# Optimization experiments

Measured on AMD Instinct MI355X. Metric: run time of the kernel, lower is better.

The kernel has to match this reference:

```python
import jax, jax.numpy as jnp
import numpy as np

H = 512
L = 4
A = 16
EPS = 1e-5


def setup_inputs() -> dict:
    key = jax.random.key(0)
    ks = jax.random.split(key, 16)
    B, S = 64, 256
    scale = 0.02
    inp = {
        "hidden": jnp.zeros((B, H), jnp.float32),
        "x": jax.random.normal(ks[0], (B, S, H), jnp.float32),
        "dones": jax.random.randint(ks[1], (B, S), 0, 2).astype(bool),
        "avail_actions": jax.random.randint(ks[2], (B, S, A), 0, 2).astype(bool),
        # MLP stack: L layers of Linear(H,H) + LayerNorm
        "Wl": jax.random.normal(ks[3], (L, H, H), jnp.float32) * scale,
        "bl": jnp.zeros((L, H), jnp.float32),
        "ln_g": jnp.ones((L, H), jnp.float32),
        "ln_b": jnp.zeros((L, H), jnp.float32),
        # GRUCell(H, H): torch layout weight_ih [3H, H] (r, z, n order)
        "W_ih": jax.random.normal(ks[4], (3 * H, H), jnp.float32) * scale,
        "W_hh": jax.random.normal(ks[5], (3 * H, H), jnp.float32) * scale,
        "b_ih": jnp.zeros((3 * H,), jnp.float32),
        "b_hh": jnp.zeros((3 * H,), jnp.float32),
        # output head
        "Wq": jax.random.normal(ks[6], (A, H), jnp.float32) * scale,
        "bq": jnp.zeros((A,), jnp.float32),
    }
    return inp


def _layer_norm(x, g, b):
    mu = jnp.mean(x, axis=-1, keepdims=True)
    var = jnp.mean(jnp.square(x - mu), axis=-1, keepdims=True)
    return (x - mu) * jax.lax.rsqrt(var + EPS) * g + b


def _gru_scan(h0, x, dones, W_ih, W_hh, b_ih, b_hh):
    # Precompute input projections for all timesteps: [B, S, 3H]
    gi = jnp.einsum("bsh,gh->bsg", x, W_ih) + b_ih
    gi_t = jnp.swapaxes(gi, 0, 1)          # [S, B, 3H]
    dones_t = jnp.swapaxes(dones, 0, 1)    # [S, B]

    def step(h, inputs):
        gi_s, done_s = inputs
        h = jnp.where(done_s[:, None], 0.0, h)  # reset carry where done
        gh = h @ W_hh.T + b_hh
        i_r, i_z, i_n = jnp.split(gi_s, 3, axis=-1)
        h_r, h_z, h_n = jnp.split(gh, 3, axis=-1)
        r = jax.nn.sigmoid(i_r + h_r)
        z = jax.nn.sigmoid(i_z + h_z)
        n = jnp.tanh(i_n + r * h_n)
        h_new = (1.0 - z) * n + z * h
        return h_new, h_new

    h_final, outs = jax.lax.scan(step, h0, (gi_t, dones_t))
    return h_final, jnp.swapaxes(outs, 0, 1)  # [B, S, H]


def reference(hidden, x, dones, avail_actions, Wl, bl, ln_g, ln_b,
              W_ih, W_hh, b_ih, b_hh, Wq, bq):
    h = x
    for l in range(L):
        h = jnp.einsum("bsh,oh->bso", h, Wl[l]) + bl[l]
        h = jax.nn.relu(_layer_norm(h, ln_g[l], ln_b[l]))
    hidden_out, rnn_out = _gru_scan(hidden, h, dones, W_ih, W_hh, b_ih, b_hh)
    q = jnp.einsum("bsh,ah->bsa", rnn_out, Wq) + bq
    unavail = 1.0 - avail_actions.astype(q.dtype)
    q = q - unavail * 1e10
    return hidden_out, q
```

## Files before the change

### kernel.cpp

```cpp
#include <hip/hip_runtime.h>
#include <hip/hip_bf16.h>

typedef short short8 __attribute__((ext_vector_type(8)));
typedef float f32x4 __attribute__((ext_vector_type(4)));

#define H 512
#define BATCH 64
#define SEQ 256
#define NROWS 16384
#define NDOM 16
#define HSTCAP 12288

__device__ __forceinline__ float bf2f(unsigned short u) {
    union { unsigned int i; float f; } v;
    v.i = ((unsigned int)u) << 16;
    return v.f;
}
__device__ __forceinline__ unsigned short f2bf(float f) {
    union { float f; unsigned int i; } v;
    v.f = f;
    unsigned int lsb = (v.i >> 16) & 1u;
    v.i += 0x7fffu + lsb;
    return (unsigned short)(v.i >> 16);
}
__device__ __forceinline__ float sigm(float x) { return 1.f / (1.f + __expf(-x)); }
__device__ __forceinline__ float tanh_fast(float x) { return 2.f / (1.f + __expf(-2.f * x)) - 1.f; }

__global__ __launch_bounds__(256) void cvt_init(
    const float* __restrict__ Wl, const float* __restrict__ Wih,
    unsigned short* __restrict__ wlb, unsigned short* __restrict__ wihb,
    unsigned int* __restrict__ meta)
{
    long idx4 = (long)blockIdx.x * 256 + threadIdx.x;
    if (idx4 < 20480) meta[idx4] = 0u;
    long i = idx4 * 4;
    const long N1 = 1048576;
    const long N2 = N1 + 786432;
    const float* src; unsigned short* dst; long off;
    if (i < N1)      { src = Wl;  dst = wlb;  off = i; }
    else if (i < N2) { src = Wih; dst = wihb; off = i - N1; }
    else return;
    float4 v = *(const float4*)(src + off);
    ushort4 o;
    o.x = f2bf(v.x); o.y = f2bf(v.y); o.z = f2bf(v.z); o.w = f2bf(v.w);
    *(ushort4*)(dst + off) = o;
}

__global__ __launch_bounds__(256) void seg_build(
    const int* __restrict__ dones, int* __restrict__ lenArr,
    unsigned int* __restrict__ hist)
{
    __shared__ int d[256];
    const int b = blockIdx.x, s = threadIdx.x;
    d[s] = dones[b * 256 + s];
    __syncthreads();
    int len = 0;
    bool start = (s == 0) || (d[s] != 0);
    if (start) {
        len = 1;
        while (s + len < 256 && d[s + len] == 0) len++;
        atomicAdd(&hist[len], 1u);
    }
    lenArr[b * 256 + s] = len;
}

__global__ __launch_bounds__(256) void seg_offsets(
    const unsigned int* __restrict__ hist, int* __restrict__ Marr,
    unsigned int* __restrict__ offs, unsigned int* __restrict__ ssum)
{
    __shared__ unsigned int h[257];
    __shared__ int Msh[257];
    const int t = threadIdx.x;
    h[t] = hist[t];
    if (t == 0) h[256] = hist[256];
    __syncthreads();
    for (int tt = t; tt <= 256; tt += 256) {
        unsigned int m = 0;
        for (int L = tt + 1; L <= 256; ++L) m += h[L];
        Marr[tt] = (int)m;
        offs[tt] = m;
        Msh[tt] = (int)m;
    }
    __syncthreads();
    if (t == 0) {
        unsigned int acc = 0;
        for (int k = 0; k <= 256; ++k) { ssum[k] = acc; acc += (unsigned int)Msh[k]; }
    }
}

__global__ __launch_bounds__(256) void seg_scatter(
    const int* __restrict__ lenArr, unsigned int* __restrict__ offs,
    int* __restrict__ recs)
{
    const int b = blockIdx.x, s = threadIdx.x;
    int len = lenArr[b * 256 + s];
    if (len > 0) {
        unsigned int pos = atomicAdd(&offs[len], 1u);
        recs[pos] = (b << 16) | s;
    }
}

__global__ __launch_bounds__(256) void pmap_build(
    const int* __restrict__ recs, const int* __restrict__ Marr,
    const unsigned int* __restrict__ ssum, const int* __restrict__ lenArr,
    int* __restrict__ pmap)
{
    const int i = blockIdx.x * 256 + threadIdx.x;
    if (i >= Marr[0]) return;
    int rec = recs[i];
    int b = rec >> 16, st = rec & 0xffff;
    int len = lenArr[b * 256 + st];
    for (int t = 0; t < len; ++t) pmap[b * 256 + st + t] = (int)ssum[t] + i;
}

__global__ __launch_bounds__(256) void h_init(
    const int* __restrict__ recs, const int* __restrict__ Marr,
    const int* __restrict__ dones, const float* __restrict__ hidden,
    unsigned short* __restrict__ hst)
{
    const int w = threadIdx.x >> 6, lane = threadIdx.x & 63;
    const int i = blockIdx.x * 4 + w;
    const int nseg = Marr[0];
    const int c0 = lane * 8;
    unsigned short* dst = hst + (long)i * 512 + c0;
    if (i < nseg) {
        int rec = recs[i];
        int b = rec >> 16, st = rec & 0xffff;
        if (st == 0 && dones[b * 256] == 0) {
            float4 va = *(const float4*)(hidden + b * 512 + c0);
            float4 vb = *(const float4*)(hidden + b * 512 + c0 + 4);
            ushort4 o0 = {f2bf(va.x), f2bf(va.y), f2bf(va.z), f2bf(va.w)};
            ushort4 o1 = {f2bf(vb.x), f2bf(vb.y), f2bf(vb.z), f2bf(vb.w)};
            *(ushort4*)dst = o0; *(ushort4*)(dst + 4) = o1;
            return;
        }
    }
    ushort4 z4 = {0, 0, 0, 0};
    *(ushort4*)dst = z4; *(ushort4*)(dst + 4) = z4;
}

__global__ __launch_bounds__(256, 2) void mlp_gi(
    const float* __restrict__ x,
    const unsigned short* __restrict__ wlb,
    const unsigned short* __restrict__ wihb,
    const float* __restrict__ bl,
    const float* __restrict__ lng,
    const float* __restrict__ lnb,
    const float* __restrict__ bih,
    const int* __restrict__ pmap,
    unsigned short* __restrict__ gi)
{
    __shared__ unsigned short ldsAct[32 * 512];
    __shared__ unsigned short ldsW[512 * 32];
    __shared__ float red[32 * 8];
    const int tid = threadIdx.x;
    const int lane = tid & 63;
    const int w = tid >> 6;
    const long m0 = (long)blockIdx.x * 32;
    const int l15 = lane & 15;
    const int l4 = lane >> 4;

    int stSrc[8];
    unsigned int* stDst[8];
#pragma unroll
    for (int i = 0; i < 8; ++i) {
        int o = (i * 256 + tid) * 16;
        int row = o >> 6;
        int ch = (o & 63) >> 4;
        int sw = (row & 3) ^ ((row >> 2) & 3);
        stSrc[i] = row * 1024 + ((ch ^ sw) << 4);
        stDst[i] = (unsigned int*)(ldsW + (i * 256 + w * 64) * 8);
    }
    int afBase[2], afSw[2];
#pragma unroll
    for (int i = 0; i < 2; ++i) {
        int arow = i * 16 + l15;
        afBase[i] = arow * 1024 + l4 * 16;
        afSw[i] = (arow & 7) << 4;
    }
    int bfOff[8];
#pragma unroll
    for (int jn = 0; jn < 8; ++jn) {
        int wrow = w * 128 + jn * 16 + l15;
        int sw = (wrow & 3) ^ ((wrow >> 2) & 3);
        bfOff[jn] = wrow * 64 + ((l4 ^ sw) << 4);
    }

#pragma unroll
    for (int it = 0; it < 8; ++it) {
        int ch = it * 256 + tid;
        int row = ch >> 6;
        int c = ch & 63;
        const float* xp = x + (m0 + row) * 512 + c * 8;
        float4 a = *(const float4*)xp;
        float4 b4 = *(const float4*)(xp + 4);
        short8 v;
        v[0] = (short)f2bf(a.x);  v[1] = (short)f2bf(a.y);
        v[2] = (short)f2bf(a.z);  v[3] = (short)f2bf(a.w);
        v[4] = (short)f2bf(b4.x); v[5] = (short)f2bf(b4.y);
        v[6] = (short)f2bf(b4.z); v[7] = (short)f2bf(b4.w);
        int byteo = (row * 1024 + c * 16) ^ ((row & 7) << 4);
        *(short8*)((char*)ldsAct + byteo) = v;
    }
    __syncthreads();

    for (int u = 0; u < 7; ++u) {
        const char* Wb = (u < 4) ? (const char*)(wlb + (long)u * 262144)
                                 : (const char*)(wihb + (long)(u - 4) * 262144);
        f32x4 acc[2][8];
#pragma unroll
        for (int i = 0; i < 2; ++i)
#pragma unroll
            for (int jn = 0; jn < 8; ++jn) acc[i][jn] = (f32x4){0.f, 0.f, 0.f, 0.f};

        for (int kt = 0; kt < 16; ++kt) {
            const int ktb = kt * 64;
            __syncthreads();
#pragma unroll
            for (int i = 0; i < 8; ++i)
                __builtin_amdgcn_global_load_lds(
                    (const unsigned int*)(Wb + stSrc[i] + ktb), stDst[i], 16, 0, 0);
            __syncthreads();

            short8 af[2], bfr[8];
#pragma unroll
            for (int i = 0; i < 2; ++i)
                af[i] = *(const short8*)((const char*)ldsAct + ((afBase[i] + ktb) ^ afSw[i]));
#pragma unroll
            for (int jn = 0; jn < 8; ++jn)
                bfr[jn] = *(const short8*)((const char*)ldsW + bfOff[jn]);
            __builtin_amdgcn_s_setprio(1);
#pragma unroll
            for (int i = 0; i < 2; ++i)
#pragma unroll
                for (int jn = 0; jn < 8; ++jn)
                    acc[i][jn] = __builtin_amdgcn_mfma_f32_16x16x32_bf16(af[i], bfr[jn], acc[i][jn], 0, 0, 0);
            __builtin_amdgcn_s_setprio(0);
        }

        if (u < 4) {
            float bz[8], gl[8], bb[8];
#pragma unroll
            for (int jn = 0; jn < 8; ++jn) {
                int n = w * 128 + jn * 16 + l15;
                bz[jn] = bl[u * 512 + n]; gl[jn] = lng[u * 512 + n]; bb[jn] = lnb[u * 512 + n];
            }
#pragma unroll
            for (int i = 0; i < 2; ++i)
#pragma unroll
                for (int jn = 0; jn < 8; ++jn)
#pragma unroll
                    for (int r = 0; r < 4; ++r) acc[i][jn][r] += bz[jn];

#pragma unroll
            for (int i = 0; i < 2; ++i) {
#pragma unroll
                for (int r = 0; r < 4; ++r) {
                    float sv = 0.f, qv = 0.f;
#pragma unroll
                    for (int jn = 0; jn < 8; ++jn) {
                        float v = acc[i][jn][r];
                        sv += v; qv += v * v;
                    }
                    sv += __shfl_xor(sv, 1); qv += __shfl_xor(qv, 1);
                    sv += __shfl_xor(sv, 2); qv += __shfl_xor(qv, 2);
                    sv += __shfl_xor(sv, 4); qv += __shfl_xor(qv, 4);
                    sv += __shfl_xor(sv, 8); qv += __shfl_xor(qv, 8);
                    if (l15 == 0) {
                        int row = i * 16 + l4 * 4 + r;
                        red[row * 8 + w * 2] = sv;
                        red[row * 8 + w * 2 + 1] = qv;
                    }
                }
            }
            __syncthreads();

#pragma unroll
            for (int i = 0; i < 2; ++i) {
#pragma unroll
                for (int r = 0; r < 4; ++r) {
                    int row = i * 16 + l4 * 4 + r;
                    float s_tot = red[row * 8 + 0] + red[row * 8 + 2] + red[row * 8 + 4] + red[row * 8 + 6];
                    float q_tot = red[row * 8 + 1] + red[row * 8 + 3] + red[row * 8 + 5] + red[row * 8 + 7];
                    float mu = s_tot * (1.f / 512.f);
                    float var = q_tot * (1.f / 512.f) - mu * mu;
                    float rs = rsqrtf(var + 1e-5f);
#pragma unroll
                    for (int jn = 0; jn < 8; ++jn) {
                        int col = w * 128 + jn * 16 + l15;
                        float v = fmaxf(0.f, (acc[i][jn][r] - mu) * rs * gl[jn] + bb[jn]);
                        int byteo = (row * 1024 + col * 2) ^ ((row & 7) << 4);
                        *(unsigned short*)((char*)ldsAct + byteo) = f2bf(v);
                    }
                }
            }
            __syncthreads();
        } else {
            const int nc = u - 4;
            __syncthreads();
#pragma unroll
            for (int jn = 0; jn < 8; ++jn) {
                int colg = nc * 512 + w * 128 + jn * 16 + l15;
                float bz = bih[colg];
#pragma unroll
                for (int i = 0; i < 2; ++i)
#pragma unroll
                    for (int r = 0; r < 4; ++r) {
                        int row = i * 16 + l4 * 4 + r;
                        int col = w * 128 + jn * 16 + l15;
                        int byteo = (row * 1024 + col * 2) ^ ((row & 7) << 4);
                        *(unsigned short*)((char*)ldsW + byteo) = f2bf(acc[i][jn][r] + bz);
                    }
            }
            __syncthreads();
#pragma unroll
            for (int k = 0; k < 8; ++k) {
                int row = w * 8 + k;
                int pmr = pmap[m0 + row];
                int byteo = (row * 1024 + lane * 16) ^ ((row & 7) << 4);
                short8 v = *(const short8*)((const char*)ldsW + byteo);
                *(short8*)(gi + (long)pmr * 1536 + nc * 512 + lane * 8) = v;
            }
        }
    }
}

__device__ __forceinline__ void dbar(unsigned int* __restrict__ dm,
                                     int wg, unsigned int epoch)
{
    __syncthreads();
    const int tid = threadIdx.x;
    if (wg == 0) {
        if (tid == 0)
            __hip_atomic_store(&dm[0], epoch + 1u, __ATOMIC_RELAXED,
                               __HIP_MEMORY_SCOPE_AGENT);
        if (tid < 16) {
            while (__hip_atomic_load(&dm[tid * 32], __ATOMIC_RELAXED,
                                     __HIP_MEMORY_SCOPE_AGENT) <= epoch)
                __builtin_amdgcn_s_sleep(1);
        }
        if (tid == 0)
            __hip_atomic_store(&dm[512], epoch + 1u, __ATOMIC_RELAXED,
                               __HIP_MEMORY_SCOPE_AGENT);
    } else {
        if (tid == 0) {
            __hip_atomic_store(&dm[wg * 32], epoch + 1u, __ATOMIC_RELAXED,
                               __HIP_MEMORY_SCOPE_AGENT);
            while (__hip_atomic_load(&dm[512], __ATOMIC_RELAXED,
                                     __HIP_MEMORY_SCOPE_AGENT) <= epoch)
                __builtin_amdgcn_s_sleep(1);
        }
    }
    __syncthreads();
    __builtin_amdgcn_sched_barrier(0);
}

__global__ __launch_bounds__(256, 1) void gru_seg_scan(
    const unsigned short* __restrict__ gi,
    const float* __restrict__ Whh,
    const float* __restrict__ bhh,
    const int* __restrict__ Marr,
    const unsigned int* __restrict__ ssum,
    const int* __restrict__ recs,
    unsigned short* __restrict__ hstA,
    unsigned short* __restrict__ hstB,
    unsigned short* __restrict__ rnn,
    float* __restrict__ hid_out,
    unsigned int* __restrict__ meta)
{
    __shared__ unsigned short ldsW[96 * 512];
    __shared__ int sMarr[257];
    __shared__ unsigned int sssum[257];
    const int tid = threadIdx.x;
    const int lane = tid & 63;
    const int w = tid >> 6;
    const int jg = blockIdx.x >> 4;
    const int dom = blockIdx.x & 15;
    const int j0 = jg * 32;

    for (int e = tid; e < 96 * 512; e += 256) {
        int rrow = e >> 9;
        int col = e & 511;
        int gate = rrow >> 5;
        int jl = rrow & 31;
        float v = Whh[((long)(gate * 512 + j0 + jl)) * 512 + col];
        int byteo = (rrow * 1024 + col * 2) ^ ((rrow & 7) << 4);
        *(unsigned short*)((char*)ldsW + byteo) = f2bf(v);
    }
    for (int e = tid; e < 257; e += 256) { sMarr[e] = Marr[e]; sssum[e] = ssum[e]; }

    const int jl16 = lane & 15;
    float bhr[2], bhz[2], bhn[2];
#pragma unroll
    for (int jj = 0; jj < 2; ++jj) {
        int jc = j0 + jj * 16 + jl16;
        bhr[jj] = bhh[jc]; bhz[jj] = bhh[512 + jc]; bhn[jj] = bhh[1024 + jc];
    }
    const int rbase = w * 16 + (lane >> 4) * 4;
    const int arowl = w * 16 + jl16;
    const int kcol0 = (lane >> 4) * 8;
    unsigned int* dmeta = meta + 1024 * dom;
    __syncthreads();

    int crec[4], nrec[4];
    unsigned short cgr[4][2], cgz[4][2], cgn[4][2];
    unsigned short ngr[4][2], ngz[4][2], ngn[4][2];

    {
        const int Mt0 = sMarr[0];
        const long b0 = (long)sssum[0];
#pragma unroll
        for (int q = 0; q < 4; ++q) {
            int r = dom * 64 + rbase + q;
            if (r < Mt0) {
                crec[q] = recs[r];
#pragma unroll
                for (int jj = 0; jj < 2; ++jj) {
                    const unsigned short* gp = gi + (b0 + r) * 1536 + j0 + jj * 16 + jl16;
                    cgr[q][jj] = gp[0]; cgz[q][jj] = gp[512]; cgn[q][jj] = gp[1024];
                }
            } else crec[q] = -1;
        }
    }

    for (int t = 0; t < 256; ++t) {
        const int Mt = sMarr[t];
        if (Mt == 0) break;
        const int ntiles = (Mt + 63) >> 6;
        if (dom >= ntiles) break;
        const unsigned short* hsrc = (t & 1) ? hstB : hstA;
        unsigned short* hdst = (t & 1) ? hstA : hstB;
        const long base = (long)sssum[t];

        for (int tt = dom; tt < ntiles; tt += NDOM) {
            const int r0 = tt * 64;

            const unsigned short* arowp = hsrc + ((long)(r0 + arowl)) * 512 + kcol0;
            short8 af[16];
#pragma unroll
            for (int kk = 0; kk < 16; ++kk) {
                const unsigned short* ap = arowp + kk * 32;
                asm volatile("global_load_dwordx4 %0, %1, off sc0"
                             : "=v"(af[kk]) : "v"(ap));
            }
            unsigned int hu[4][2];
#pragma unroll
            for (int q = 0; q < 4; ++q)
#pragma unroll
                for (int jj = 0; jj < 2; ++jj) {
                    const unsigned short* hp = hsrc + (long)(r0 + rbase + q) * 512
                                             + j0 + jj * 16 + jl16;
                    asm volatile("global_load_ushort %0, %1, off sc0"
                                 : "=v"(hu[q][jj]) : "v"(hp));
                }
            asm volatile("s_waitcnt vmcnt(0)" ::: "memory");
            __builtin_amdgcn_sched_barrier(0);

            const bool instep = (tt + NDOM < ntiles);
            if (instep) {
#pragma unroll
                for (int q = 0; q < 4; ++q) {
                    int r = (tt + NDOM) * 64 + rbase + q;
                    if (r < Mt) {
                        nrec[q] = recs[r];
#pragma unroll
                        for (int jj = 0; jj < 2; ++jj) {
                            const unsigned short* gp = gi + (base + r) * 1536 + j0 + jj * 16 + jl16;
                            ngr[q][jj] = gp[0]; ngz[q][jj] = gp[512]; ngn[q][jj] = gp[1024];
                        }
                    } else nrec[q] = -1;
                }
            }

            f32x4 acch[3][2];
#pragma unroll
            for (int g = 0; g < 3; ++g)
#pragma unroll
                for (int jj = 0; jj < 2; ++jj) acch[g][jj] = (f32x4){0.f, 0.f, 0.f, 0.f};

#pragma unroll
            for (int kk = 0; kk < 16; ++kk) {
#pragma unroll
                for (int g = 0; g < 3; ++g)
#pragma unroll
                    for (int jj = 0; jj < 2; ++jj) {
                        int rrow = g * 32 + jj * 16 + jl16;
                        int bbyte = (rrow * 1024 + kk * 64 + ((lane >> 4) * 16)) ^ ((rrow & 7) << 4);
                        short8 bfrag = *(const short8*)((const char*)ldsW + bbyte);
                        acch[g][jj] = __builtin_amdgcn_mfma_f32_16x16x32_bf16(af[kk], bfrag, acch[g][jj], 0, 0, 0);
                    }
            }

#pragma unroll
            for (int q = 0; q < 4; ++q) {
                if (crec[q] >= 0) {
                    int r = r0 + rbase + q;
                    int b = crec[q] >> 16, st = crec[q] & 0xffff;
                    int s = st + t;
#pragma unroll
                    for (int jj = 0; jj < 2; ++jj) {
                        int jc = j0 + jj * 16 + jl16;
                        float heff = bf2f((unsigned short)hu[q][jj]);
                        float rgt = sigm(bf2f(cgr[q][jj]) + acch[0][jj][q] + bhr[jj]);
                        float zgt = sigm(bf2f(cgz[q][jj]) + acch[1][jj][q] + bhz[jj]);
                        float ngt = tanh_fast(bf2f(cgn[q][jj]) + rgt * (acch[2][jj][q] + bhn[jj]));
                        float hnew = (1.f - zgt) * ngt + zgt * heff;
                        unsigned short hb16 = f2bf(hnew);
                        hdst[(long)r * 512 + jc] = hb16;
                        rnn[((long)(b * 256 + s)) * 512 + jc] = hb16;
                        if (s == 255) hid_out[b * 512 + jc] = hnew;
                    }
                }
            }
            if (instep) {
#pragma unroll
                for (int q = 0; q < 4; ++q) {
                    crec[q] = nrec[q];
#pragma unroll
                    for (int jj = 0; jj < 2; ++jj) {
                        cgr[q][jj] = ngr[q][jj]; cgz[q][jj] = ngz[q][jj]; cgn[q][jj] = ngn[q][jj];
                    }
                }
            }
        }

        {
            const int Mt1 = sMarr[t + 1];
            if (Mt1 > 0 && dom < ((Mt1 + 63) >> 6)) {
                const long b1 = (long)sssum[t + 1];
#pragma unroll
                for (int q = 0; q < 4; ++q) {
                    int r = dom * 64 + rbase + q;
                    if (r < Mt1) {
                        crec[q] = recs[r];
#pragma unroll
                        for (int jj = 0; jj < 2; ++jj) {
                            const unsigned short* gp = gi + (b1 + r) * 1536 + j0 + jj * 16 + jl16;
                            cgr[q][jj] = gp[0]; cgz[q][jj] = gp[512]; cgn[q][jj] = gp[1024];
                        }
                    } else crec[q] = -1;
                }
            }
        }
        dbar(dmeta, jg, (unsigned int)t);
    }
}

__global__ __launch_bounds__(256) void qhead(
    const unsigned short* __restrict__ rnn, const float* __restrict__ Wq,
    const float* __restrict__ bq, const int* __restrict__ avail,
    float* __restrict__ qout)
{
    const int w = threadIdx.x >> 6;
    const int lane = threadIdx.x & 63;
    const long row = (long)blockIdx.x * 4 + w;
    const int a = lane & 15;
    const int kc = lane >> 4;
    const unsigned short* hr = rnn + row * H + kc * 128;
    const float* wr = Wq + a * H + kc * 128;
    float sum = 0.f;
#pragma unroll
    for (int i = 0; i < 128; i += 8) {
        short8 hv = *(const short8*)(hr + i);
        float4 wa = *(const float4*)(wr + i);
        float4 wb = *(const float4*)(wr + i + 4);
        sum += bf2f((unsigned short)hv[0]) * wa.x;
        sum += bf2f((unsigned short)hv[1]) * wa.y;
        sum += bf2f((unsigned short)hv[2]) * wa.z;
        sum += bf2f((unsigned short)hv[3]) * wa.w;
        sum += bf2f((unsigned short)hv[4]) * wb.x;
        sum += bf2f((unsigned short)hv[5]) * wb.y;
        sum += bf2f((unsigned short)hv[6]) * wb.z;
        sum += bf2f((unsigned short)hv[7]) * wb.w;
    }
    sum += __shfl_xor(sum, 16);
    sum += __shfl_xor(sum, 32);
    if (kc == 0) {
        float qv = sum + bq[a];
        int av = avail[row * 16 + a];
        if (av == 0) qv -= 1e10f;
        qout[row * 16 + a] = qv;
    }
}

extern "C" void kernel_launch(void* const* d_in, const int* in_sizes, int n_in,
                              void* d_out, int out_size, void* d_ws, size_t ws_size,
                              hipStream_t stream)
{
    const float* hidden = (const float*)d_in[0];
    const float* x      = (const float*)d_in[1];
    const int*   dones  = (const int*)d_in[2];
    const int*   avail  = (const int*)d_in[3];
    const float* Wl     = (const float*)d_in[4];
    const float* bl     = (const float*)d_in[5];
    const float* ln_g   = (const float*)d_in[6];
    const float* ln_b   = (const float*)d_in[7];
    const float* W_ih   = (const float*)d_in[8];
    const float* W_hh   = (const float*)d_in[9];
    const float* b_ih   = (const float*)d_in[10];
    const float* b_hh   = (const float*)d_in[11];
    const float* Wq     = (const float*)d_in[12];
    const float* bq     = (const float*)d_in[13];

    char* p = (char*)d_ws;
    unsigned short* gi   = (unsigned short*)p; p += (size_t)NROWS * 1536 * 2;
    unsigned short* rnn  = (unsigned short*)p; p += (size_t)NROWS * H * 2;
    unsigned short* hst0 = (unsigned short*)p; p += (size_t)HSTCAP * H * 2;
    unsigned short* hst1 = (unsigned short*)p; p += (size_t)HSTCAP * H * 2;
    unsigned short* wlb  = (unsigned short*)p; p += (size_t)4 * H * H * 2;
    unsigned short* wihb = (unsigned short*)p; p += (size_t)3 * H * H * 2;
    int* lenArr = (int*)p;          p += (size_t)NROWS * 4;
    int* recs   = (int*)p;          p += (size_t)NROWS * 4;
    int* pmap   = (int*)p;          p += (size_t)NROWS * 4;
    unsigned int* meta = (unsigned int*)p;  p += 20480 * 4;
    unsigned int* hist = meta + 16384;
    unsigned int* offs = meta + 16672;
    int* Marr = (int*)(meta + 16960);
    unsigned int* ssum = meta + 17248;

    cvt_init<<<1792, 256, 0, stream>>>(Wl, W_ih, wlb, wihb, meta);

    seg_build<<<64, 256, 0, stream>>>(dones, lenArr, hist);
    seg_offsets<<<1, 256, 0, stream>>>(hist, Marr, offs, ssum);
    seg_scatter<<<64, 256, 0, stream>>>(lenArr, offs, recs);
    pmap_build<<<64, 256, 0, stream>>>(recs, Marr, ssum, lenArr, pmap);

    h_init<<<HSTCAP / 4, 256, 0, stream>>>(recs, Marr, dones, hidden, hst0);

    mlp_gi<<<512, 256, 0, stream>>>(x, wlb, wihb, bl, ln_g, ln_b, b_ih, pmap, gi);

    gru_seg_scan<<<256, 256, 0, stream>>>(gi, W_hh, b_hh, Marr, ssum, recs,
                                          hst0, hst1, rnn, (float*)d_out, meta);

    qhead<<<4096, 256, 0, stream>>>(rnn, Wq, bq, avail, (float*)d_out + BATCH * H);
}
```

Measured before the change: 613.9 us.

## Double-buffer weight tiles in MLP/GI kernel and keep activations in registers

The weight K-tiles in the fused MLP+input-projection kernel now go through two LDS buffers, with global-to-LDS loads issued two tiles ahead and gated by explicit vmcnt waits and raw barriers. Previously each K step did a load, sync and compute in series. The 32-row activation tile is loaded once per layer into registers (af[2][16]), so the separate activation LDS array goes away and buffer 0 is reused as scratch. This is meant to overlap weight fetch latency with MFMA work, at the cost of higher register pressure from the 32 short8 activation fragments and more delicate synchronization.

```diff
diff --git a/kernel.cpp b/kernel.cpp
--- a/kernel.cpp
+++ b/kernel.cpp
@@ -150,8 +150,7 @@
     const int* __restrict__ pmap,
     unsigned short* __restrict__ gi)
 {
-    __shared__ unsigned short ldsAct[32 * 512];
-    __shared__ unsigned short ldsW[512 * 32];
+    __shared__ unsigned short ldsW[2][512 * 32];
     __shared__ float red[32 * 8];
     const int tid = threadIdx.x;
     const int lane = tid & 63;
@@ -159,17 +158,20 @@
     const long m0 = (long)blockIdx.x * 32;
     const int l15 = lane & 15;
     const int l4 = lane >> 4;
-
-    int stSrc[8];
-    unsigned int* stDst[8];
-#pragma unroll
-    for (int i = 0; i < 8; ++i) {
-        int o = (i * 256 + tid) * 16;
-        int row = o >> 6;
-        int ch = (o & 63) >> 4;
-        int sw = (row & 3) ^ ((row >> 2) & 3);
-        stSrc[i] = row * 1024 + ((ch ^ sw) << 4);
-        stDst[i] = (unsigned int*)(ldsW + (i * 256 + w * 64) * 8);
+    char* scratch = (char*)&ldsW[0][0];
+
+    const int rowb = tid >> 2;
+    const int chb = tid & 3;
+    const int swb = (rowb & 3) ^ ((rowb >> 2) & 3);
+    const int srcBase = rowb * 1024 + ((chb ^ swb) << 4);
+    const int dstBase = w * 1024;
+
+    int bfOff[8];
+#pragma unroll
+    for (int jn = 0; jn < 8; ++jn) {
+        int wrow = w * 128 + jn * 16 + l15;
+        int sw = (wrow & 3) ^ ((wrow >> 2) & 3);
+        bfOff[jn] = wrow * 64 + ((l4 ^ sw) << 4);
     }
     int afBase[2], afSw[2];
 #pragma unroll
@@ -178,12 +180,15 @@
         afBase[i] = arow * 1024 + l4 * 16;
         afSw[i] = (arow & 7) << 4;
     }
-    int bfOff[8];
-#pragma unroll
-    for (int jn = 0; jn < 8; ++jn) {
-        int wrow = w * 128 + jn * 16 + l15;
-        int sw = (wrow & 3) ^ ((wrow >> 2) & 3);
-        bfOff[jn] = wrow * 64 + ((l4 ^ sw) << 4);
+
+#define STAGE(SL, BUF)                                                        \
+    {                                                                         \
+        _Pragma("unroll")                                                     \
+        for (int i_ = 0; i_ < 8; ++i_)                                        \
+            __builtin_amdgcn_global_load_lds(                                 \
+                (const unsigned int*)(Wb + srcBase + i_ * 65536 + (SL) * 64), \
+                (unsigned int*)((char*)&ldsW[(BUF)][0] + dstBase + i_ * 4096),\
+                16, 0, 0);                                                    \
     }
 
 #pragma unroll
@@ -200,8 +205,15 @@
         v[4] = (short)f2bf(b4.x); v[5] = (short)f2bf(b4.y);
         v[6] = (short)f2bf(b4.z); v[7] = (short)f2bf(b4.w);
         int byteo = (row * 1024 + c * 16) ^ ((row & 7) << 4);
-        *(short8*)((char*)ldsAct + byteo) = v;
-    }
+        *(short8*)(scratch + byteo) = v;
+    }
+    __syncthreads();
+    short8 af[2][16];
+#pragma unroll
+    for (int i = 0; i < 2; ++i)
+#pragma unroll
+        for (int kt = 0; kt < 16; ++kt)
+            af[i][kt] = *(const short8*)(scratch + ((afBase[i] + kt * 64) ^ afSw[i]));
     __syncthreads();
 
     for (int u = 0; u < 7; ++u) {
@@ -213,30 +225,31 @@
 #pragma unroll
             for (int jn = 0; jn < 8; ++jn) acc[i][jn] = (f32x4){0.f, 0.f, 0.f, 0.f};
 
+        STAGE(0, 0)
+        STAGE(1, 1)
+#pragma unroll
         for (int kt = 0; kt < 16; ++kt) {
-            const int ktb = kt * 64;
-            __syncthreads();
-#pragma unroll
-            for (int i = 0; i < 8; ++i)
-                __builtin_amdgcn_global_load_lds(
-                    (const unsigned int*)(Wb + stSrc[i] + ktb), stDst[i], 16, 0, 0);
-            __syncthreads();
-
-            short8 af[2], bfr[8];
+            if (kt < 15) asm volatile("s_waitcnt vmcnt(8)" ::: "memory");
+            else         asm volatile("s_waitcnt vmcnt(0)" ::: "memory");
+            __builtin_amdgcn_sched_barrier(0);
+            __builtin_amdgcn_s_barrier();
+            __builtin_amdgcn_sched_barrier(0);
+            const char* wbuf = (const char*)&ldsW[kt & 1][0];
+            short8 bfr[8];
+#pragma unroll
+            for (int jn = 0; jn < 8; ++jn)
+                bfr[jn] = *(const short8*)(wbuf + bfOff[jn]);
 #pragma unroll
             for (int i = 0; i < 2; ++i)
-                af[i] = *(const short8*)((const char*)ldsAct + ((afBase[i] + ktb) ^ afSw[i]));
-#pragma unroll
-            for (int jn = 0; jn < 8; ++jn)
-                bfr[jn] = *(const short8*)((const char*)ldsW + bfOff[jn]);
-            __builtin_amdgcn_s_setprio(1);
-#pragma unroll
-            for (int i = 0; i < 2; ++i)
 #pragma unroll
                 for (int jn = 0; jn < 8; ++jn)
-                    acc[i][jn] = __builtin_amdgcn_mfma_f32_16x16x32_bf16(af[i], bfr[jn], acc[i][jn], 0, 0, 0);
-            __builtin_amdgcn_s_setprio(0);
-        }
+                    acc[i][jn] = __builtin_amdgcn_mfma_f32_16x16x32_bf16(af[i][kt], bfr[jn], acc[i][jn], 0, 0, 0);
+            __builtin_amdgcn_sched_barrier(0);
+            __builtin_amdgcn_s_barrier();
+            __builtin_amdgcn_sched_barrier(0);
+            if (kt < 14) STAGE(kt + 2, kt & 1)
+        }
+        __syncthreads();
 
         if (u < 4) {
             float bz[8], gl[8], bb[8];
@@ -290,14 +303,19 @@
                         int col = w * 128 + jn * 16 + l15;
                         float v = fmaxf(0.f, (acc[i][jn][r] - mu) * rs * gl[jn] + bb[jn]);
                         int byteo = (row * 1024 + col * 2) ^ ((row & 7) << 4);
-                        *(unsigned short*)((char*)ldsAct + byteo) = f2bf(v);
+                        *(unsigned short*)(scratch + byteo) = f2bf(v);
                     }
                 }
             }
+            __syncthreads();
+#pragma unroll
+            for (int i = 0; i < 2; ++i)
+#pragma unroll
+                for (int kt = 0; kt < 16; ++kt)
+                    af[i][kt] = *(const short8*)(scratch + ((afBase[i] + kt * 64) ^ afSw[i]));
             __syncthreads();
         } else {
             const int nc = u - 4;
-            __syncthreads();
 #pragma unroll
             for (int jn = 0; jn < 8; ++jn) {
                 int colg = nc * 512 + w * 128 + jn * 16 + l15;
@@ -309,7 +327,7 @@
                         int row = i * 16 + l4 * 4 + r;
                         int col = w * 128 + jn * 16 + l15;
                         int byteo = (row * 1024 + col * 2) ^ ((row & 7) << 4);
-                        *(unsigned short*)((char*)ldsW + byteo) = f2bf(acc[i][jn][r] + bz);
+                        *(unsigned short*)(scratch + byteo) = f2bf(acc[i][jn][r] + bz);
                     }
             }
             __syncthreads();
@@ -318,11 +336,13 @@
                 int row = w * 8 + k;
                 int pmr = pmap[m0 + row];
                 int byteo = (row * 1024 + lane * 16) ^ ((row & 7) << 4);
-                short8 v = *(const short8*)((const char*)ldsW + byteo);
+                short8 v = *(const short8*)(scratch + byteo);
                 *(short8*)(gi + (long)pmr * 1536 + nc * 512 + lane * 8) = v;
             }
-        }
-    }
+            __syncthreads();
+        }
+    }
+#undef STAGE
 }
 
 __device__ __forceinline__ void dbar(unsigned int* __restrict__ dm,
```

Result: slower. 663.5 us (+8.1%).
